# Performance work log

Hardware: AMD Instinct MI355X
Metric: run time of the kernel (lower is better)

Reference implementation:

```python
import jax, jax.numpy as jnp
import numpy as np

N_NODES = 100000
N_EDGES = 6400000
N_FEAT = 128
HIDDEN = 16
OUT = 2
N_GRAPHS = 64


def setup_inputs() -> dict:
    key = jax.random.key(0)
    ks = jax.random.split(key, 8)
    x = jax.random.normal(ks[0], (N_NODES, N_FEAT), dtype=jnp.float32)
    edge_index = jax.random.randint(ks[1], (2, N_EDGES), 0, N_NODES, dtype=jnp.int64)
    batch_idx = jnp.sort(jax.random.randint(ks[2], (N_NODES,), 0, N_GRAPHS, dtype=jnp.int64))
    # GCNConv params (Glorot-ish scale)
    W1 = jax.random.normal(ks[3], (N_FEAT, HIDDEN), dtype=jnp.float32) / np.sqrt(N_FEAT)
    b1 = jnp.zeros((HIDDEN,), dtype=jnp.float32)
    prelu_a = jnp.full((1,), 0.25, dtype=jnp.float32)  # torch.nn.PReLU default
    W2 = jax.random.normal(ks[4], (HIDDEN, OUT), dtype=jnp.float32) / np.sqrt(HIDDEN)
    b2 = jnp.zeros((OUT,), dtype=jnp.float32)
    return {"x": x, "W1": W1, "b1": b1, "prelu_a": prelu_a, "W2": W2, "b2": b2,
            "edge_index": edge_index, "batch_idx": batch_idx}


def _gcn_conv(h, W, b, src, dst, norm, n_nodes):
    h = h @ W                                  # [N, d_out]
    msg = h[src] * norm[:, None]               # gather + normalize, [E', d_out]
    agg = jax.ops.segment_sum(msg, dst, num_segments=n_nodes)  # scatter-add
    return agg + b


def reference(x, W1, b1, prelu_a, W2, b2, edge_index, batch_idx):
    n_nodes = x.shape[0]
    # GCNConv default: add self-loops, symmetric normalization D^-1/2 A D^-1/2
    loops = jnp.arange(n_nodes, dtype=edge_index.dtype)
    src = jnp.concatenate([edge_index[0], loops])
    dst = jnp.concatenate([edge_index[1], loops])
    deg = jax.ops.segment_sum(jnp.ones_like(dst, dtype=x.dtype), dst, num_segments=n_nodes)
    dinv = jnp.where(deg > 0, jax.lax.rsqrt(deg), 0.0)
    norm = dinv[src] * dinv[dst]               # [E']

    h = _gcn_conv(x, W1, b1, src, dst, norm, n_nodes)
    h = jnp.where(h >= 0, h, prelu_a * h)      # PReLU (single shared slope)
    h = _gcn_conv(h, W2, b2, src, dst, norm, n_nodes)

    # global mean pool over graphs
    sums = jax.ops.segment_sum(h, batch_idx, num_segments=N_GRAPHS)
    cnts = jax.ops.segment_sum(jnp.ones((n_nodes,), dtype=h.dtype), batch_idx, num_segments=N_GRAPHS)
    return sums / jnp.maximum(cnts, 1.0)[:, None]
```

## Files before the change

### kernel.cpp

```cpp
#include <hip/hip_runtime.h>

#define NFEAT 128
#define HID 16
#define NOUT 2
#define NGRAPH 64

#define BN 196
#define NBUCK 512
#define NCB 512
#define CH 12500
#define EPT 13
#define CAP 13824
#define PSTRIDE 192
#define WST 132
#define ACST 9

#define S20F 1048576.0f
#define S20I 9.5367431640625e-7f
#define S18F 262144.0f
#define S18I 3.814697265625e-6f
#define SPF  32768.0f
#define SPI  3.0517578125e-5f
#define OFF23 0x800000
#define OFF22 0x400000

typedef unsigned short ushortv8 __attribute__((ext_vector_type(8)));
typedef float fvec4 __attribute__((ext_vector_type(4)));

__device__ __forceinline__ int chunk_id(int bid) { return ((bid & 7) << 6) | (bid >> 3); }

__device__ __forceinline__ unsigned short f2bf(float f) {
    unsigned u = __float_as_uint(f);
    return (unsigned short)((u + 0x7FFFu + ((u >> 16) & 1u)) >> 16);
}

__device__ __forceinline__ float bf2f(unsigned short b) {
    return __uint_as_float(((unsigned)b) << 16);
}

__device__ __forceinline__ unsigned bucket_of(int d) { return (unsigned)d / (unsigned)BN; }

__global__ __launch_bounds__(1024) void k_scatter(const int* __restrict__ src, const int* __restrict__ dst,
                                                  int* __restrict__ cursor,
                                                  unsigned int* __restrict__ bpk, int E) {
    __shared__ unsigned int stage[CH + 44];
    __shared__ int hist4[4 * NBUCK];
    __shared__ int scan[512];
    __shared__ int excl[NBUCK + 1];
    __shared__ int cur[NBUCK];
    int t = threadIdx.x;
    int cid = chunk_id(blockIdx.x);
    int start = cid * CH;
    int end = min(E, start + CH);
    for (int i = t; i < 4 * NBUCK; i += 1024) hist4[i] = 0;
    __syncthreads();

    unsigned int w[EPT];
    int kb[EPT];
    int rep = (t & 3) * NBUCK;
    #pragma unroll
    for (int i = 0; i < EPT; i++) {
        int e = start + i * 1024 + t;
        kb[i] = -1;
        if (e < end) {
            int s = __builtin_nontemporal_load(src + e);
            int d = __builtin_nontemporal_load(dst + e);
            unsigned b = bucket_of(d);
            int dl = d - (int)(b * BN);
            kb[i] = (int)b;
            w[i] = ((unsigned)dl << 17) | (unsigned)s;
            atomicAdd(&hist4[rep + (int)b], 1);
        }
    }
    __syncthreads();

    int hc = 0, gb = 0;
    if (t < NBUCK) {
        hc = hist4[t] + hist4[NBUCK + t] + hist4[2 * NBUCK + t] + hist4[3 * NBUCK + t];
        if (hc > 0) gb = atomicAdd(&cursor[t], hc);
    }
    if (t < 512) scan[t] = (t < NBUCK) ? hc : 0;
    __syncthreads();
    for (int off = 1; off < 512; off <<= 1) {
        int a = 0;
        if (t < 512 && t >= off) a = scan[t - off];
        __syncthreads();
        if (t < 512 && t >= off) scan[t] += a;
        __syncthreads();
    }
    if (t < NBUCK) {
        int ex = scan[t] - hc;
        excl[t] = ex;
        cur[t] = ex;
        hist4[t] = gb;
    }
    if (t == 0) excl[NBUCK] = end - start;
    __syncthreads();

    #pragma unroll
    for (int i = 0; i < EPT; i++) {
        if (kb[i] >= 0) {
            int r = atomicAdd(&cur[kb[i]], 1);
            stage[r] = w[i];
        }
    }
    __syncthreads();

    int wave = t >> 6, lane = t & 63;
    for (int b = wave; b < NBUCK; b += 16) {
        int s0 = excl[b], s1 = excl[b + 1];
        int run = s1 - s0;
        if (run <= 0) continue;
        int gbase = hist4[b];
        int avail = CAP - gbase;
        int lim = min(run, max(avail, 0));
        for (int j = lane; j < lim; j += 64)
            bpk[(size_t)b * CAP + gbase + j] = stage[s0 + j];
    }
}

__global__ __launch_bounds__(1024) void k_degw1(const unsigned int* __restrict__ bpk, const int* __restrict__ cursor,
                                                const float* __restrict__ x, const float* __restrict__ W1,
                                                int* __restrict__ deg, float* __restrict__ dinv,
                                                unsigned short* __restrict__ h1b, int N) {
    __shared__ int hdeg[BN];
    __shared__ float sdinv[BN];
    __shared__ float sWT[HID * WST];
    __shared__ float sx[64 * 132];
    int t = threadIdx.x;
    int k = blockIdx.x;
    if (t < BN) hdeg[t] = 0;
    for (int i = t; i < HID * NFEAT; i += 1024) {
        int h = i >> 7, kk = i & 127;
        sWT[h * WST + kk] = W1[kk * HID + h];
    }
    __syncthreads();
    int bstart = k * CAP;
    int bend = bstart + cursor[k];
    for (int e = bstart + t; e < bend; e += 1024)
        atomicAdd(&hdeg[__builtin_nontemporal_load(bpk + e) >> 17], 1);
    __syncthreads();
    if (t < BN) {
        int gn = k * BN + t;
        float di = rsqrtf(1.0f + (float)hdeg[t]);
        sdinv[t] = di;
        if (gn < N) { deg[gn] = hdeg[t]; dinv[gn] = di; }
    }
    __syncthreads();

    int local = t >> 4;
    int h     = t & 15;
    for (int nb = 0; nb < 4; nb++) {
        int ln = nb * 64 + local;
        int gn = k * BN + ln;
        bool valid = (ln < BN) && (gn < N);
        if (valid) {
            const fvec4* xr = (const fvec4*)(x + (size_t)gn * NFEAT);
            fvec4 a = __builtin_nontemporal_load(xr + h * 2);
            fvec4 b = __builtin_nontemporal_load(xr + h * 2 + 1);
            float* sp = sx + local * 132 + h * 8;
            ((fvec4*)sp)[0] = a;
            ((fvec4*)sp)[1] = b;
        }
        __syncthreads();
        if (valid) {
            const fvec4* xr4 = (const fvec4*)(sx + local * 132);
            const fvec4* wr4 = (const fvec4*)(sWT + h * WST);
            float acc = 0.0f;
            #pragma unroll
            for (int k4 = 0; k4 < 32; k4++) {
                fvec4 a = xr4[k4];
                fvec4 b = wr4[k4];
                acc += a.x * b.x + a.y * b.y + a.z * b.z + a.w * b.w;
            }
            h1b[(size_t)gn * HID + h] = f2bf(acc * sdinv[ln]);
        }
        __syncthreads();
    }
}

__global__ __launch_bounds__(1024) void k_bg1(const unsigned int* __restrict__ bpk, const int* __restrict__ cursor,
                                              const unsigned short* __restrict__ h1b, const float* __restrict__ dinv,
                                              const int* __restrict__ deg,
                                              const float* __restrict__ b1, const float* __restrict__ prelu_a,
                                              const float* __restrict__ W2,
                                              float* __restrict__ t2s, int N) {
    __shared__ unsigned long long acc[BN * ACST];
    int t = threadIdx.x;
    int k = blockIdx.x;
    for (int i = t; i < BN * ACST; i += 1024) acc[i] = 0ull;
    __syncthreads();
    int bstart = k * CAP;
    int bend = bstart + cursor[k];
    int q = t & 1;
    const uint4* h4 = (const uint4*)h1b;

    int e = bstart + (t >> 1);
    unsigned int w = (e < bend) ? __builtin_nontemporal_load(bpk + e) : 0u;
    while (e < bend) {
        int e2 = e + 512;
        unsigned int wn = (e2 < bend) ? __builtin_nontemporal_load(bpk + e2) : 0u;
        int d = (int)(w >> 17);
        int s = (int)(w & 0x1FFFFu);
        uint4 u = h4[(size_t)s * 2 + q];
        unsigned long long* ap = acc + d * ACST + q * 4;
        #pragma unroll
        for (int jj = 0; jj < 4; jj++) {
            unsigned uu = (&u.x)[jj];
            float flo = __uint_as_float((uu << 16) + 0x0A000000u);
            float fhi = __uint_as_float((uu & 0xFFFF0000u) + 0x0A000000u);
            unsigned lo = (unsigned)(__float2int_rn(flo) + OFF23);
            unsigned hi = (unsigned)(__float2int_rn(fhi) + OFF23);
            atomicAdd(&ap[jj], ((unsigned long long)hi << 32) | (unsigned long long)lo);
        }
        w = wn;
        e = e2;
    }
    __syncthreads();

    if (t < BN * 2) {
        int n = t >> 1;
        int qq = t & 1;
        int gn = k * BN + n;
        if (gn < N) {
            float di = dinv[gn];
            int dg = deg[gn];
            long long bias = (long long)dg << 23;
            float a = prelu_a[0];
            const ushortv8* h8 = (const ushortv8*)h1b;
            ushortv8 sv = h8[(size_t)gn * 2 + qq];
            float o0 = 0.0f, o1 = 0.0f;
            #pragma unroll
            for (int jj = 0; jj < 4; jj++) {
                unsigned long long av = acc[n * ACST + qq * 4 + jj];
                float f0 = (float)((long long)(unsigned)av - bias) * S20I;
                float f1 = (float)((long long)(av >> 32) - bias) * S20I;
                int fa = qq * 8 + 2 * jj;
                float tv = di * (f0 + bf2f(sv[2 * jj])) + b1[fa];
                tv = (tv >= 0.0f) ? tv : a * tv;
                o0 += tv * W2[fa * 2 + 0];
                o1 += tv * W2[fa * 2 + 1];
                int fb = fa + 1;
                float tw = di * (f1 + bf2f(sv[2 * jj + 1])) + b1[fb];
                tw = (tw >= 0.0f) ? tw : a * tw;
                o0 += tw * W2[fb * 2 + 0];
                o1 += tw * W2[fb * 2 + 1];
            }
            o0 += __shfl_xor(o0, 1);
            o1 += __shfl_xor(o1, 1);
            if (qq == 0)
                *(float2*)(t2s + (size_t)gn * 2) = make_float2(di * o0, di * o1);
        }
    }
}

__global__ __launch_bounds__(1024) void k_bg2(const unsigned int* __restrict__ bpk, const int* __restrict__ cursor,
                                              const float* __restrict__ t2s, const float* __restrict__ dinv,
                                              const int* __restrict__ deg, const int* __restrict__ batch,
                                              int* __restrict__ bins, int N) {
    __shared__ unsigned long long acc2[BN];
    __shared__ int pg[PSTRIDE];
    int t = threadIdx.x;
    int k = blockIdx.x;
    if (t < BN) acc2[t] = 0ull;
    if (t < PSTRIDE) pg[t] = 0;
    __syncthreads();
    int bstart = k * CAP;
    int bend = bstart + cursor[k];

    int e = bstart + t;
    unsigned int w = (e < bend) ? __builtin_nontemporal_load(bpk + e) : 0u;
    while (e < bend) {
        int e2 = e + 1024;
        unsigned int wn = (e2 < bend) ? __builtin_nontemporal_load(bpk + e2) : 0u;
        int d = (int)(w >> 17);
        int s = (int)(w & 0x1FFFFu);
        float2 v = *(const float2*)(t2s + (size_t)s * 2);
        unsigned lo = (unsigned)(__float2int_rn(v.x * S18F) + OFF22);
        unsigned hi = (unsigned)(__float2int_rn(v.y * S18F) + OFF22);
        atomicAdd(&acc2[d], ((unsigned long long)hi << 32) | (unsigned long long)lo);
        w = wn;
        e = e2;
    }
    __syncthreads();
    if (t < BN) {
        int gn = k * BN + t;
        if (gn < N) {
            float dd = dinv[gn];
            int dg = deg[gn];
            long long bias = (long long)dg << 22;
            unsigned long long av = acc2[t];
            float2 self = *(const float2*)(t2s + (size_t)gn * 2);
            float v0 = (float)((long long)(unsigned)av - bias) * S18I + self.x;
            float v1 = (float)((long long)(av >> 32) - bias) * S18I + self.y;
            int g = batch[gn];
            atomicAdd(&pg[g * 2 + 0], __float2int_rn(dd * v0 * SPF));
            atomicAdd(&pg[g * 2 + 1], __float2int_rn(dd * v1 * SPF));
            atomicAdd(&pg[128 + g], 1);
        }
    }
    __syncthreads();
    if (t < PSTRIDE && pg[t] != 0) atomicAdd(&bins[t], pg[t]);
}

__global__ __launch_bounds__(128) void k_final(const int* __restrict__ bins,
                                               const float* __restrict__ b2, float* __restrict__ out) {
    int t = threadIdx.x;
    if (t < NGRAPH * NOUT) {
        int g = t >> 1, c = t & 1;
        float cnt = (float)bins[128 + g];
        float val = (float)bins[t] * SPI;
        out[t] = (val + cnt * b2[c]) / fmaxf(cnt, 1.0f);
    }
}

extern "C" void kernel_launch(void* const* d_in, const int* in_sizes, int n_in,
                              void* d_out, int out_size, void* d_ws, size_t ws_size,
                              hipStream_t stream) {
    const float* x       = (const float*)d_in[0];
    const float* W1      = (const float*)d_in[1];
    const float* b1      = (const float*)d_in[2];
    const float* prelu_a = (const float*)d_in[3];
    const float* W2      = (const float*)d_in[4];
    const float* b2      = (const float*)d_in[5];
    const int*   ei      = (const int*)d_in[6];
    const int*   batch   = (const int*)d_in[7];

    const int N = in_sizes[7];
    const int E = in_sizes[6] / 2;
    const int* src = ei;
    const int* dst = ei + E;

    float* ws     = (float*)d_ws;
    float* dinv   = ws;
    int*   deg    = (int*)(dinv + 100352);
    unsigned short* h1b = (unsigned short*)(deg + 100352);
    float* t2s    = (float*)((int*)h1b + 802816);
    int*   cursor = (int*)(t2s + 200064);
    int*   bins   = cursor + 512;
    unsigned int* bpk = (unsigned int*)(bins + 256);

    float* out = (float*)d_out;

    hipMemsetAsync(cursor, 0, (512 + 256) * sizeof(int), stream);
    k_scatter<<<NCB, 1024, 0, stream>>>(src, dst, cursor, bpk, E);
    k_degw1<<<NBUCK, 1024, 0, stream>>>(bpk, cursor, x, W1, deg, dinv, h1b, N);
    k_bg1<<<NBUCK, 1024, 0, stream>>>(bpk, cursor, h1b, dinv, deg, b1, prelu_a, W2, t2s, N);
    k_bg2<<<NBUCK, 1024, 0, stream>>>(bpk, cursor, t2s, dinv, deg, batch, bins, N);
    k_final<<<1, 128, 0, stream>>>(bins, b2, out);
}
```

Measured before the change: 256.5 us.

## Store h1 as int16 fixed-point, wave-shuffle scan, fuse final pooling via ticket

Replaces the bf16 storage of the first-layer hidden features with 12-bit-fraction int16 fixed point. The layer-1 aggregation can then add integer lanes directly into the packed 64-bit shared atomics instead of converting float to int per element. The block scan in the scatter kernel now uses wave shuffles plus per-wave sums in place of a shared-memory Hillis-Steele loop with many barriers. The final mean-pool kernel is folded into the last block of k_bg2 through a global ticket counter, which saves one launch. The int16 scale clamps values at about ±8 and has coarser resolution than before, so accuracy may suffer if hidden values exceed that range.

```diff
diff --git a/kernel.cpp b/kernel.cpp
--- a/kernel.cpp
+++ b/kernel.cpp
@@ -15,28 +15,19 @@
 #define WST 132
 #define ACST 9
 
-#define S20F 1048576.0f
-#define S20I 9.5367431640625e-7f
+#define S12F 4096.0f
+#define S12I 2.44140625e-4f
+#define OFF15 32768
 #define S18F 262144.0f
 #define S18I 3.814697265625e-6f
 #define SPF  32768.0f
 #define SPI  3.0517578125e-5f
-#define OFF23 0x800000
 #define OFF22 0x400000
 
 typedef unsigned short ushortv8 __attribute__((ext_vector_type(8)));
 typedef float fvec4 __attribute__((ext_vector_type(4)));
 
 __device__ __forceinline__ int chunk_id(int bid) { return ((bid & 7) << 6) | (bid >> 3); }
-
-__device__ __forceinline__ unsigned short f2bf(float f) {
-    unsigned u = __float_as_uint(f);
-    return (unsigned short)((u + 0x7FFFu + ((u >> 16) & 1u)) >> 16);
-}
-
-__device__ __forceinline__ float bf2f(unsigned short b) {
-    return __uint_as_float(((unsigned)b) << 16);
-}
 
 __device__ __forceinline__ unsigned bucket_of(int d) { return (unsigned)d / (unsigned)BN; }
 
@@ -45,7 +36,7 @@
                                                   unsigned int* __restrict__ bpk, int E) {
     __shared__ unsigned int stage[CH + 44];
     __shared__ int hist4[4 * NBUCK];
-    __shared__ int scan[512];
+    __shared__ int wsum[8];
     __shared__ int excl[NBUCK + 1];
     __shared__ int cur[NBUCK];
     int t = threadIdx.x;
@@ -79,17 +70,20 @@
         hc = hist4[t] + hist4[NBUCK + t] + hist4[2 * NBUCK + t] + hist4[3 * NBUCK + t];
         if (hc > 0) gb = atomicAdd(&cursor[t], hc);
     }
-    if (t < 512) scan[t] = (t < NBUCK) ? hc : 0;
-    __syncthreads();
-    for (int off = 1; off < 512; off <<= 1) {
-        int a = 0;
-        if (t < 512 && t >= off) a = scan[t - off];
-        __syncthreads();
-        if (t < 512 && t >= off) scan[t] += a;
-        __syncthreads();
-    }
+    int lane = t & 63;
+    int wv = t >> 6;
+    int sv_ = hc;
+    #pragma unroll
+    for (int off = 1; off < 64; off <<= 1) {
+        int o = __shfl_up(sv_, off);
+        if (lane >= off) sv_ += o;
+    }
+    if (t < 512 && lane == 63) wsum[wv] = sv_;
+    __syncthreads();
     if (t < NBUCK) {
-        int ex = scan[t] - hc;
+        int woff = 0;
+        for (int i = 0; i < wv; i++) woff += wsum[i];
+        int ex = (sv_ + woff) - hc;
         excl[t] = ex;
         cur[t] = ex;
         hist4[t] = gb;
@@ -106,7 +100,7 @@
     }
     __syncthreads();
 
-    int wave = t >> 6, lane = t & 63;
+    int wave = t >> 6;
     for (int b = wave; b < NBUCK; b += 16) {
         int s0 = excl[b], s1 = excl[b + 1];
         int run = s1 - s0;
@@ -173,7 +167,8 @@
                 fvec4 b = wr4[k4];
                 acc += a.x * b.x + a.y * b.y + a.z * b.z + a.w * b.w;
             }
-            h1b[(size_t)gn * HID + h] = f2bf(acc * sdinv[ln]);
+            float hv = fminf(fmaxf(acc * sdinv[ln] * S12F, -32767.0f), 32767.0f);
+            ((short*)h1b)[(size_t)gn * HID + h] = (short)__float2int_rn(hv);
         }
         __syncthreads();
     }
@@ -207,10 +202,8 @@
         #pragma unroll
         for (int jj = 0; jj < 4; jj++) {
             unsigned uu = (&u.x)[jj];
-            float flo = __uint_as_float((uu << 16) + 0x0A000000u);
-            float fhi = __uint_as_float((uu & 0xFFFF0000u) + 0x0A000000u);
-            unsigned lo = (unsigned)(__float2int_rn(flo) + OFF23);
-            unsigned hi = (unsigned)(__float2int_rn(fhi) + OFF23);
+            unsigned lo = (unsigned)((int)(short)(uu & 0xFFFFu) + OFF15);
+            unsigned hi = (unsigned)(((int)uu >> 16) + OFF15);
             atomicAdd(&ap[jj], ((unsigned long long)hi << 32) | (unsigned long long)lo);
         }
         w = wn;
@@ -225,7 +218,7 @@
         if (gn < N) {
             float di = dinv[gn];
             int dg = deg[gn];
-            long long bias = (long long)dg << 23;
+            long long bias = (long long)dg << 15;
             float a = prelu_a[0];
             const ushortv8* h8 = (const ushortv8*)h1b;
             ushortv8 sv = h8[(size_t)gn * 2 + qq];
@@ -233,15 +226,17 @@
             #pragma unroll
             for (int jj = 0; jj < 4; jj++) {
                 unsigned long long av = acc[n * ACST + qq * 4 + jj];
-                float f0 = (float)((long long)(unsigned)av - bias) * S20I;
-                float f1 = (float)((long long)(av >> 32) - bias) * S20I;
+                float f0 = (float)((long long)(unsigned)av - bias) * S12I;
+                float f1 = (float)((long long)(av >> 32) - bias) * S12I;
                 int fa = qq * 8 + 2 * jj;
-                float tv = di * (f0 + bf2f(sv[2 * jj])) + b1[fa];
+                float s0 = (float)(short)sv[2 * jj] * S12I;
+                float tv = di * (f0 + s0) + b1[fa];
                 tv = (tv >= 0.0f) ? tv : a * tv;
                 o0 += tv * W2[fa * 2 + 0];
                 o1 += tv * W2[fa * 2 + 1];
                 int fb = fa + 1;
-                float tw = di * (f1 + bf2f(sv[2 * jj + 1])) + b1[fb];
+                float s1 = (float)(short)sv[2 * jj + 1] * S12I;
+                float tw = di * (f1 + s1) + b1[fb];
                 tw = (tw >= 0.0f) ? tw : a * tw;
                 o0 += tw * W2[fb * 2 + 0];
                 o1 += tw * W2[fb * 2 + 1];
@@ -257,9 +252,12 @@
 __global__ __launch_bounds__(1024) void k_bg2(const unsigned int* __restrict__ bpk, const int* __restrict__ cursor,
                                               const float* __restrict__ t2s, const float* __restrict__ dinv,
                                               const int* __restrict__ deg, const int* __restrict__ batch,
-                                              int* __restrict__ bins, int N) {
+                                              const float* __restrict__ b2,
+                                              int* __restrict__ bins, unsigned int* __restrict__ ticket,
+                                              float* __restrict__ out, int N) {
     __shared__ unsigned long long acc2[BN];
     __shared__ int pg[PSTRIDE];
+    __shared__ int lastFlag;
     int t = threadIdx.x;
     int k = blockIdx.x;
     if (t < BN) acc2[t] = 0ull;
@@ -301,15 +299,20 @@
     }
     __syncthreads();
     if (t < PSTRIDE && pg[t] != 0) atomicAdd(&bins[t], pg[t]);
-}
-
-__global__ __launch_bounds__(128) void k_final(const int* __restrict__ bins,
-                                               const float* __restrict__ b2, float* __restrict__ out) {
-    int t = threadIdx.x;
-    if (t < NGRAPH * NOUT) {
+
+    __threadfence();
+    __syncthreads();
+    if (t == 0) {
+        unsigned tk = __hip_atomic_fetch_add(ticket, 1u, __ATOMIC_ACQ_REL, __HIP_MEMORY_SCOPE_AGENT);
+        lastFlag = (tk == (unsigned)(NBUCK - 1));
+    }
+    __syncthreads();
+    if (lastFlag && t < NGRAPH * NOUT) {
         int g = t >> 1, c = t & 1;
-        float cnt = (float)bins[128 + g];
-        float val = (float)bins[t] * SPI;
+        int ci = __hip_atomic_load(&bins[128 + g], __ATOMIC_RELAXED, __HIP_MEMORY_SCOPE_AGENT);
+        int vi = __hip_atomic_load(&bins[t], __ATOMIC_RELAXED, __HIP_MEMORY_SCOPE_AGENT);
+        float cnt = (float)ci;
+        float val = (float)vi * SPI;
         out[t] = (val + cnt * b2[c]) / fmaxf(cnt, 1.0f);
     }
 }
@@ -338,14 +341,14 @@
     float* t2s    = (float*)((int*)h1b + 802816);
     int*   cursor = (int*)(t2s + 200064);
     int*   bins   = cursor + 512;
-    unsigned int* bpk = (unsigned int*)(bins + 256);
+    unsigned int* ticket = (unsigned int*)(bins + 256);
+    unsigned int* bpk = (unsigned int*)(bins + 272);
 
     float* out = (float*)d_out;
 
-    hipMemsetAsync(cursor, 0, (512 + 256) * sizeof(int), stream);
+    hipMemsetAsync(cursor, 0, (512 + 256 + 16) * sizeof(int), stream);
     k_scatter<<<NCB, 1024, 0, stream>>>(src, dst, cursor, bpk, E);
     k_degw1<<<NBUCK, 1024, 0, stream>>>(bpk, cursor, x, W1, deg, dinv, h1b, N);
     k_bg1<<<NBUCK, 1024, 0, stream>>>(bpk, cursor, h1b, dinv, deg, b1, prelu_a, W2, t2s, N);
-    k_bg2<<<NBUCK, 1024, 0, stream>>>(bpk, cursor, t2s, dinv, deg, batch, bins, N);
-    k_final<<<1, 128, 0, stream>>>(bins, b2, out);
-}
+    k_bg2<<<NBUCK, 1024, 0, stream>>>(bpk, cursor, t2s, dinv, deg, batch, b2, bins, ticket, out, N);
+}
```

New measurement: 411.1 us. 1.6x slower.
